# Kernel optimization log

Hardware: AMD Instinct MI355X
Metric: run time of the kernel (lower is better)

## Reference

```python
import jax, jax.numpy as jnp
import numpy as np

# --- configuration (matches init_kwargs) ---
T0 = 0.0; T1 = 7776000.0          # 90 days, seconds
DT = 60.0                          # Euler step
DT_FORCING = 3600.0                # hourly forcing
DTK = 864000.0                     # 10-day kernel spacing
FC = 1e-4                          # Coriolis freq
NL = 1
NDT = len(np.arange(T0, T1, DTK))          # 9 basis knots
NT = len(np.arange(T0, T1, DT_FORCING))    # 2160 forcing steps
NSUB = int(DT_FORCING // DT)               # 60 substeps
NFORCING = int((T1 - T0) // DT_FORCING)    # 2160


def setup_inputs() -> dict:
    key = jax.random.key(0)
    k1, k2, k3 = jax.random.split(key, 3)
    # K = exp(pk) ~ 1e-5: physically realistic, Euler-stable damping
    pk = (-11.5 + 0.1 * jax.random.normal(k1, (NDT * 2 * NL,))).astype(jnp.float32)
    TAx = (1e-5 * jax.random.normal(k2, (NT,))).astype(jnp.float32)
    TAy = (1e-5 * jax.random.normal(k3, (NT,))).astype(jnp.float32)
    return {"pk": pk, "TAx": TAx, "TAy": TAy}


def _pkt2Kt_matrix():
    # Gaussian basis interpolation matrix (NT, NDT), rows normalized to sum 1.
    gtime = jnp.arange(T0, T1, DT_FORCING, dtype=jnp.float32)
    gptime = jnp.arange(T0, T1, DTK, dtype=jnp.float32)
    d = (gtime[:, None] - gptime[None, :]) / DTK
    M = jnp.exp(-0.5 * d * d)
    return M / jnp.sum(M, axis=1, keepdims=True)


def _gradient(x, dx):
    # jnp.gradient along axis 0 with scalar spacing dx (central diff, one-sided ends)
    interior = (x[2:] - x[:-2]) / (2.0 * dx)
    left = ((x[1] - x[0]) / dx)[None]
    right = ((x[-1] - x[-2]) / dx)[None]
    return jnp.concatenate([left, interior, right])


def reference(pk, TAx, TAy):
    K = jnp.exp(pk).reshape(NDT, 2 * NL)          # kt_1D_to_2D
    Kt = _pkt2Kt_matrix() @ K                      # (NT, 2)
    T = TAx + 1j * TAy
    Ce = Kt[:, 0] * T / (Kt[:, 1] + 1j * FC)       # Ekman current
    Ue, Ve = jnp.real(Ce), jnp.imag(Ce)
    dCedt = _gradient(Ce, DT)                      # original uses dt spacing
    dUedt, dVedt = jnp.real(dCedt), jnp.imag(dCedt)

    def vector_field(t, U, V):
        it = (t // DT).astype(jnp.int32)
        itf = it // NSUB
        aa = jnp.mod(it, NSUB) / NSUB
        itsup = jnp.where(itf + 1 >= NT, -1, itf + 1)
        Ktnow = (1.0 - aa) * Kt[it - 1] + aa * Kt[itsup]   # jnp wraps/clamps like original
        dUe = (1.0 - aa) * dUedt[itf] + aa * dUedt[itsup]
        dVe = (1.0 - aa) * dVedt[itf] + aa * dVedt[itsup]
        d_U = -Ktnow[1] * U + FC * V - dUe
        d_V = -Ktnow[1] * V - FC * U - dVe
        return d_U, d_V

    def inner(carry, iin):
        U, V, iout = carry
        t = iout * DT_FORCING + iin * DT
        d_U, d_V = vector_field(t, U, V)
        return (U + DT * d_U, V + DT * d_V, iout), None

    def outer(carry, iout):
        U, V = carry
        (nU, nV, _), _ = jax.lax.scan(inner, (U[iout], V[iout], iout), jnp.arange(NSUB))
        U = U.at[iout + 1].set(nU)   # last update (index NFORCING) dropped, as in original
        V = V.at[iout + 1].set(nV)
        return (U, V), None

    U0 = jnp.zeros(NFORCING, jnp.float32)
    V0 = jnp.zeros(NFORCING, jnp.float32)
    (Unio, Vnio), _ = jax.lax.scan(outer, (U0, V0), jnp.arange(NFORCING))
    return jnp.stack([Ue + Unio, Ve + Vnio])  # (2, NT)
```

## Files before the change

kernel.cpp:

```cpp
#include <hip/hip_runtime.h>
#include <math.h>

#define NDT   9
#define NT    2160
#define NSUB  60
#define FC_F  1e-4f
#define DT_F  60.0f

#define BT     512
#define NWAVES (BT / 64)
#define W_OUT  128
#define L_TAIL 320
#define WMAX   (W_OUT + L_TAIL)
#define NBLK   ((NT + W_OUT - 1) / W_OUT)

__device__ __forceinline__ float gradw(const float* __restrict__ X, int i, int lo) {
  if (i == 0)      return (X[1 - lo]      - X[0 - lo])      * (1.0f / 60.0f);
  if (i == NT - 1) return (X[NT - 1 - lo] - X[NT - 2 - lo]) * (1.0f / 60.0f);
  return (X[i + 1 - lo] - X[i - 1 - lo]) * (1.0f / 120.0f);
}

__device__ __forceinline__ void kt_row(int t, const float* __restrict__ sEK,
                                       float& k0, float& k1) {
  float gt = (float)t * (1.0f / 240.0f);
  float w = expf(-0.5f * gt * gt);
  float r = expf(gt - 0.5f);
  float S = w, a0 = w * sEK[0], a1 = w * sEK[1];
  const float E[8] = {1.0f, 0.36787944f, 0.13533528f, 0.049787068f,
                      0.018315639f, 0.0067379470f, 0.0024787522f, 0.00091188197f};
#pragma unroll
  for (int j = 0; j < 8; ++j) {
    w *= r * E[j];
    S += w;
    a0 = fmaf(w, sEK[2 * (j + 1)],     a0);
    a1 = fmaf(w, sEK[2 * (j + 1) + 1], a1);
  }
  k0 = a0 / S; k1 = a1 / S;
}

__global__ __launch_bounds__(BT) void fused_slab_kernel(
    const float* __restrict__ pk,
    const float* __restrict__ TAx,
    const float* __restrict__ TAy,
    float* __restrict__ out) {
  __shared__ float  sKt1[NT];
  __shared__ float  sUe[WMAX + 3];
  __shared__ float  sVe[WMAX + 3];
  __shared__ float4 sHc[WMAX];
  __shared__ double sW[NWAVES][4];
  __shared__ float  sEK[2 * NDT];

  const int tid  = threadIdx.x;
  const int lane = tid & 63;
  const int wid  = tid >> 6;
  const int b    = blockIdx.x;

  const int out0 = b * W_OUT;
  const int ws_  = (out0 - L_TAIL > 0) ? (out0 - L_TAIL) : 0;
  const int we_  = (out0 + W_OUT < NT) ? (out0 + W_OUT) : NT;
  const int wlen = we_ - ws_;
  const int ulo  = (ws_ - 1 > 0) ? (ws_ - 1) : 0;
  const int uhi  = (we_ + 1 < NT - 1) ? (we_ + 1) : (NT - 1);
  const bool slow = (ws_ == 0);

  if (tid < 2 * NDT) sEK[tid] = expf(pk[tid]);
  __syncthreads();

  if (slow) {
    for (int t = tid; t < NT; t += BT) {
      float k0, k1; kt_row(t, sEK, k0, k1);
      sKt1[t] = k1;
      if (t >= ulo && t <= uhi) {
        float tax = TAx[t], tay = TAy[t];
        float den = k1 * k1 + FC_F * FC_F;
        float s = k0 / den;
        sUe[t - ulo] = s * (tax * k1 + tay * FC_F);
        sVe[t - ulo] = s * (tay * k1 - tax * FC_F);
      }
    }
  } else {
    int t = ulo + tid;
    if (t <= uhi) {
      float k0, k1; kt_row(t, sEK, k0, k1);
      sKt1[t] = k1;
      float tax = TAx[t], tay = TAy[t];
      float den = k1 * k1 + FC_F * FC_F;
      float s = k0 / den;
      sUe[t - ulo] = s * (tax * k1 + tay * FC_F);
      sVe[t - ulo] = s * (tay * k1 - tax * FC_F);
    }
    if (tid == 0 && uhi < NT - 1) {
      float k0, k1; kt_row(NT - 1, sEK, k0, k1);
      sKt1[NT - 1] = k1;
    }
  }
  __syncthreads();

  const float ci = -DT_F * FC_F;
  if (tid < wlen) {
    const int h = ws_ + tid;
    const int itsup = (h + 1 >= NT) ? (NT - 1) : (h + 1);
    const float dUa = gradw(sUe, h, ulo), dUb = gradw(sUe, itsup, ulo);
    const float dVa = gradw(sVe, h, ulo), dVb = gradw(sVe, itsup, ulo);
    const float kB = sKt1[itsup];
    const float Pr = -DT_F * dUa, Qr = dUa - dUb;
    const float Pi = -DT_F * dVa, Qi = dVa - dVb;

    float Sr[4]  = {1.f, 1.f, 1.f, 1.f}, Si_[4] = {0.f, 0.f, 0.f, 0.f};
    float T0r[4] = {0.f}, T0i[4] = {0.f}, T1r[4] = {0.f}, T1i[4] = {0.f};
    const int base = h * NSUB - 1;

#pragma unroll 5
    for (int il = 14; il >= 0; --il) {
#pragma unroll
      for (int m = 0; m < 4; ++m) {
        const int i = 15 * m + il;
        const float fi = (float)i;
        T0r[m] += Sr[m]; T0i[m] += Si_[m];
        T1r[m] = fmaf(fi, Sr[m], T1r[m]); T1i[m] = fmaf(fi, Si_[m], T1i[m]);
        int idx = base + i;
        idx = (idx < 0 || idx > NT - 1) ? (NT - 1) : idx;
        const float kA = sKt1[idx];
        const float a = 1.0f - (60.0f - fi) * kA - fi * kB;
        const float nSr = a * Sr[m] - ci * Si_[m];
        const float nSi = a * Si_[m] + ci * Sr[m];
        Sr[m] = nSr; Si_[m] = nSi;
      }
    }
    float Mr = 1.0f, Mi = 0.0f;
    float T0cr = 0.0f, T0ci = 0.0f, T1cr = 0.0f, T1ci = 0.0f;
#pragma unroll
    for (int m = 3; m >= 0; --m) {
      T0cr += Mr * T0r[m] - Mi * T0i[m];
      T0ci += Mr * T0i[m] + Mi * T0r[m];
      T1cr += Mr * T1r[m] - Mi * T1i[m];
      T1ci += Mr * T1i[m] + Mi * T1r[m];
      const float nMr = Mr * Sr[m] - Mi * Si_[m];
      const float nMi = Mr * Si_[m] + Mi * Sr[m];
      Mr = nMr; Mi = nMi;
    }
    const float Dr = (Pr * T0cr - Pi * T0ci) + (Qr * T1cr - Qi * T1ci);
    const float Di = (Pr * T0ci + Pi * T0cr) + (Qr * T1ci + Qi * T1cr);
    sHc[tid] = make_float4(Mr, Mi, Dr, Di);
  }
  __syncthreads();

  double Cr = 1.0, Ci2 = 0.0, Dr = 0.0, Di = 0.0;
  if (tid < wlen) {
    float4 e = sHc[tid];
    Cr = e.x; Ci2 = e.y; Dr = e.z; Di = e.w;
  }
  for (int s = 1; s < 64; s <<= 1) {
    double pCr = __shfl_up(Cr, s);
    double pCi = __shfl_up(Ci2, s);
    double pDr = __shfl_up(Dr, s);
    double pDi = __shfl_up(Di, s);
    if (lane >= s) {
      double nCr = Cr * pCr - Ci2 * pCi;
      double nCi = Cr * pCi + Ci2 * pCr;
      double nDr = Cr * pDr - Ci2 * pDi + Dr;
      double nDi = Cr * pDi + Ci2 * pDr + Di;
      Cr = nCr; Ci2 = nCi; Dr = nDr; Di = nDi;
    }
  }
  if (lane == 63) { sW[wid][0] = Cr; sW[wid][1] = Ci2; sW[wid][2] = Dr; sW[wid][3] = Di; }
  __syncthreads();

  double wCr = 1.0, wCi = 0.0, wDr = 0.0, wDi = 0.0;
  for (int w = 0; w < wid; ++w) {
    double er = sW[w][0], ei = sW[w][1], fr = sW[w][2], fi = sW[w][3];
    double nCr = er * wCr - ei * wCi;
    double nCi = er * wCi + ei * wCr;
    double nDr = er * wDr - ei * wDi + fr;
    double nDi = er * wDi + ei * wDr + fi;
    wCr = nCr; wCi = nCi; wDr = nDr; wDi = nDi;
  }
  double lCr = __shfl_up(Cr, 1), lCi = __shfl_up(Ci2, 1);
  double lDr = __shfl_up(Dr, 1), lDi = __shfl_up(Di, 1);
  if (lane == 0) { lCr = 1.0; lCi = 0.0; lDr = 0.0; lDi = 0.0; }
  double rDr = lCr * wDr - lCi * wDi + lDr;
  double rDi = lCr * wDi + lCi * wDr + lDi;

  if (tid < wlen) {
    int h = ws_ + tid;
    if (h >= out0) {
      out[h]      = (float)((double)sUe[h - ulo] + rDr);
      out[NT + h] = (float)((double)sVe[h - ulo] + rDi);
    }
  }
}

extern "C" void kernel_launch(void* const* d_in, const int* in_sizes, int n_in,
                              void* d_out, int out_size, void* d_ws, size_t ws_size,
                              hipStream_t stream) {
  const float* pk  = (const float*)d_in[0];
  const float* TAx = (const float*)d_in[1];
  const float* TAy = (const float*)d_in[2];
  float* out = (float*)d_out;
  fused_slab_kernel<<<NBLK, BT, 0, stream>>>(pk, TAx, TAy, out);
}
```

Baseline: 13.53 us.

## Replace full Kt table in first block with knot interpolation and constant tail

Block 0 previously evaluated the Gaussian-basis Kt row for all 2160 forcing steps, which made it the slowest block. It now evaluates Kt only at 136 knots spaced 16 apart and reads Kt during the substep loop by linear interpolation between knots. For forcing hours at or beyond 36, every substep index clamps to the last row, so that path uses the single constant Kt[NT-1] and skips the per-step lookup. The interpolation adds a small approximation error on the smooth Kt curve in exchange for removing most of the exp-heavy setup on the critical block.

```diff
diff --git a/kernel.cpp b/kernel.cpp
--- a/kernel.cpp
+++ b/kernel.cpp
@@ -13,6 +13,7 @@
 #define L_TAIL 320
 #define WMAX   (W_OUT + L_TAIL)
 #define NBLK   ((NT + W_OUT - 1) / W_OUT)
+#define NKNOT  136
 
 __device__ __forceinline__ float gradw(const float* __restrict__ X, int i, int lo) {
   if (i == 0)      return (X[1 - lo]      - X[0 - lo])      * (1.0f / 60.0f);
@@ -44,6 +45,7 @@
     const float* __restrict__ TAy,
     float* __restrict__ out) {
   __shared__ float  sKt1[NT];
+  __shared__ float  sKnot[NKNOT];
   __shared__ float  sUe[WMAX + 3];
   __shared__ float  sVe[WMAX + 3];
   __shared__ float4 sHc[WMAX];
@@ -66,19 +68,7 @@
   if (tid < 2 * NDT) sEK[tid] = expf(pk[tid]);
   __syncthreads();
 
-  if (slow) {
-    for (int t = tid; t < NT; t += BT) {
-      float k0, k1; kt_row(t, sEK, k0, k1);
-      sKt1[t] = k1;
-      if (t >= ulo && t <= uhi) {
-        float tax = TAx[t], tay = TAy[t];
-        float den = k1 * k1 + FC_F * FC_F;
-        float s = k0 / den;
-        sUe[t - ulo] = s * (tax * k1 + tay * FC_F);
-        sVe[t - ulo] = s * (tay * k1 - tax * FC_F);
-      }
-    }
-  } else {
+  {
     int t = ulo + tid;
     if (t <= uhi) {
       float k0, k1; kt_row(t, sEK, k0, k1);
@@ -89,10 +79,18 @@
       sUe[t - ulo] = s * (tax * k1 + tay * FC_F);
       sVe[t - ulo] = s * (tay * k1 - tax * FC_F);
     }
-    if (tid == 0 && uhi < NT - 1) {
+  }
+  if (slow) {
+    if (tid < NKNOT) {
+      float k0, k1; kt_row(16 * tid, sEK, k0, k1);
+      sKnot[tid] = k1;
+    } else if (tid == NKNOT) {
       float k0, k1; kt_row(NT - 1, sEK, k0, k1);
       sKt1[NT - 1] = k1;
     }
+  } else if (tid == 0 && uhi < NT - 1) {
+    float k0, k1; kt_row(NT - 1, sEK, k0, k1);
+    sKt1[NT - 1] = k1;
   }
   __syncthreads();
 
@@ -108,23 +106,43 @@
 
     float Sr[4]  = {1.f, 1.f, 1.f, 1.f}, Si_[4] = {0.f, 0.f, 0.f, 0.f};
     float T0r[4] = {0.f}, T0i[4] = {0.f}, T1r[4] = {0.f}, T1i[4] = {0.f};
-    const int base = h * NSUB - 1;
-
+
+    if (h >= 36) {
+      const float kA = sKt1[NT - 1];
 #pragma unroll 5
-    for (int il = 14; il >= 0; --il) {
-#pragma unroll
-      for (int m = 0; m < 4; ++m) {
-        const int i = 15 * m + il;
-        const float fi = (float)i;
-        T0r[m] += Sr[m]; T0i[m] += Si_[m];
-        T1r[m] = fmaf(fi, Sr[m], T1r[m]); T1i[m] = fmaf(fi, Si_[m], T1i[m]);
-        int idx = base + i;
-        idx = (idx < 0 || idx > NT - 1) ? (NT - 1) : idx;
-        const float kA = sKt1[idx];
-        const float a = 1.0f - (60.0f - fi) * kA - fi * kB;
-        const float nSr = a * Sr[m] - ci * Si_[m];
-        const float nSi = a * Si_[m] + ci * Sr[m];
-        Sr[m] = nSr; Si_[m] = nSi;
+      for (int il = 14; il >= 0; --il) {
+#pragma unroll
+        for (int m = 0; m < 4; ++m) {
+          const float fi = (float)(15 * m + il);
+          T0r[m] += Sr[m]; T0i[m] += Si_[m];
+          T1r[m] = fmaf(fi, Sr[m], T1r[m]); T1i[m] = fmaf(fi, Si_[m], T1i[m]);
+          const float a = 1.0f - (60.0f - fi) * kA - fi * kB;
+          const float nSr = a * Sr[m] - ci * Si_[m];
+          const float nSi = a * Si_[m] + ci * Sr[m];
+          Sr[m] = nSr; Si_[m] = nSi;
+        }
+      }
+    } else {
+      const int base = h * NSUB - 1;
+#pragma unroll 5
+      for (int il = 14; il >= 0; --il) {
+#pragma unroll
+        for (int m = 0; m < 4; ++m) {
+          const int i = 15 * m + il;
+          const float fi = (float)i;
+          T0r[m] += Sr[m]; T0i[m] += Si_[m];
+          T1r[m] = fmaf(fi, Sr[m], T1r[m]); T1i[m] = fmaf(fi, Si_[m], T1i[m]);
+          int idx = base + i;
+          idx = (idx < 0 || idx > NT - 1) ? (NT - 1) : idx;
+          const int j = idx >> 4;
+          const float f = (float)(idx & 15) * 0.0625f;
+          const float kj = sKnot[j];
+          const float kA = fmaf(sKnot[j + 1] - kj, f, kj);
+          const float a = 1.0f - (60.0f - fi) * kA - fi * kB;
+          const float nSr = a * Sr[m] - ci * Si_[m];
+          const float nSi = a * Si_[m] + ci * Sr[m];
+          Sr[m] = nSr; Si_[m] = nSi;
+        }
       }
     }
     float Mr = 1.0f, Mi = 0.0f;
```

After: 13.21 us. 1.02x faster.
